# Kernel optimization log

Hardware: AMD Instinct MI355X
Metric: run time of the kernel (lower is better)

Reference implementation:

```python
import jax, jax.numpy as jnp
import numpy as np

N_ATOMS = 4096
MAX_ATOMS = 100
N_WEIGHTS = MAX_ATOMS * (MAX_ATOMS + 1) // 2  # 5050


def setup_inputs() -> dict:
    key = jax.random.key(0)
    k1, k2, k3, k4 = jax.random.split(key, 4)
    coordinates = jax.random.normal(k1, (N_ATOMS, 3), dtype=jnp.float32)
    atom_ix = jax.random.randint(k2, (N_ATOMS,), 0, MAX_ATOMS, dtype=jnp.int64)
    weights = jax.random.normal(k3, (N_WEIGHTS,), dtype=jnp.float32)
    bias = jax.random.normal(k4, (1,), dtype=jnp.float32)
    return {"coordinates": coordinates, "atom_ix": atom_ix, "weights": weights, "bias": bias}


def reference(coordinates, atom_ix, weights, bias):
    # diff: [N, N, 3]
    diff = coordinates[None, :, :] - coordinates[:, None, :]
    # torch.norm with no dim -> scalar Frobenius norm of the whole tensor
    d = jnp.sqrt(jnp.sum(diff * diff))
    # torch.nan_to_num(1/d, 0.0): nan->0, +inf->finfo.max (jnp defaults match)
    reciprocal_d = jnp.nan_to_num(1.0 / d, nan=0.0)
    # pairwise index into triangular weight table: [N, N]
    ai = atom_ix[:, None]
    pairwise_atom_ix = ai * (ai + 1) // 2 + atom_ix[None, :]
    atom_weights = weights[pairwise_atom_ix]  # gather -> [N, N]
    return jnp.sum(atom_weights * reciprocal_d) + bias  # shape (1,)
```

## Files before the change

### kernel.cpp

```cpp
#include <hip/hip_runtime.h>
#include <math.h>


#define NTHREADS 1024
#define N_WAVES (NTHREADS / 64)

constexpr int N_ATOMS   = 4096;
constexpr int MAX_ATOMS = 100;

__device__ __forceinline__ float waveReduceSum(float v) {
#pragma unroll
    for (int off = 32; off > 0; off >>= 1)
        v += __shfl_down(v, off, 64);
    return v;
}

__global__ __launch_bounds__(NTHREADS)
void SimpleEnergyModel_43903155700342_kernel(
        const float* __restrict__ coords,
        const int*   __restrict__ atom_ix,
        const float* __restrict__ weights,
        const float* __restrict__ bias,
        float*       __restrict__ out)
{
    __shared__ float    s_part[N_WAVES][4];
    __shared__ float    s_w[N_WAVES];
    __shared__ unsigned s_count[MAX_ATOMS];
    __shared__ float    s_cntf[MAX_ATOMS];

    const int tid  = threadIdx.x;
    const int lane = tid & 63;
    const int wave = tid >> 6;

    for (int t = tid; t < MAX_ATOMS; t += NTHREADS) s_count[t] = 0u;
    __syncthreads();

    float sumsq = 0.f, sx = 0.f, sy = 0.f, sz = 0.f;
    for (int i = tid; i < N_ATOMS; i += NTHREADS) {
        const float x = coords[3 * i + 0];
        const float y = coords[3 * i + 1];
        const float z = coords[3 * i + 2];
        sumsq = fmaf(x, x, sumsq);
        sumsq = fmaf(y, y, sumsq);
        sumsq = fmaf(z, z, sumsq);
        sx += x; sy += y; sz += z;
        atomicAdd(&s_count[atom_ix[i]], 1u);
    }
    sumsq = waveReduceSum(sumsq);
    sx    = waveReduceSum(sx);
    sy    = waveReduceSum(sy);
    sz    = waveReduceSum(sz);
    if (lane == 0) {
        s_part[wave][0] = sumsq;
        s_part[wave][1] = sx;
        s_part[wave][2] = sy;
        s_part[wave][3] = sz;
    }
    __syncthreads();

    for (int t = tid; t < MAX_ATOMS; t += NTHREADS) s_cntf[t] = (float)s_count[t];
    __syncthreads();

    float wsum = 0.f;
    for (int idx = tid; idx < MAX_ATOMS * MAX_ATOMS; idx += NTHREADS) {
        const int a = idx / MAX_ATOMS;
        const int b = idx - a * MAX_ATOMS;
        const float cc = s_cntf[a] * s_cntf[b];
        wsum = fmaf(cc, weights[(a * (a + 1)) / 2 + b], wsum);
    }
    wsum = waveReduceSum(wsum);
    if (lane == 0) s_w[wave] = wsum;
    __syncthreads();

    if (tid == 0) {
        float tss = 0.f, tx = 0.f, ty = 0.f, tz = 0.f, tw = 0.f;
#pragma unroll
        for (int w = 0; w < N_WAVES; ++w) {
            tss += s_part[w][0];
            tx  += s_part[w][1];
            ty  += s_part[w][2];
            tz  += s_part[w][3];
            tw  += s_w[w];
        }
        const float S = 2.f * (float)N_ATOMS * tss - 2.f * (tx * tx + ty * ty + tz * tz);
        const float d = sqrtf(S);
        const float rd = (d != 0.f) ? (1.f / d) : 0.f;
        out[0] = tw * rd + bias[0];
    }
}

extern "C" void kernel_launch(void* const* d_in, const int* in_sizes, int n_in,
                              void* d_out, int out_size, void* d_ws, size_t ws_size,
                              hipStream_t stream) {
    const float* coords  = (const float*)d_in[0];
    const int*   atom_ix = (const int*)  d_in[1];
    const float* weights = (const float*)d_in[2];
    const float* bias    = (const float*)d_in[3];
    float*       out     = (float*)d_out;

    SimpleEnergyModel_43903155700342_kernel<<<1, NTHREADS, 0, stream>>>(
        coords, atom_ix, weights, bias, out);
}
```

Baseline: 9.763 us.

## Prefetch weight table into registers and vectorize coordinate and index loads

All ten weight-table gathers per thread are issued up front into registers, before the count histogram and coordinate reduction. This overlaps their global-memory latency with the other loads instead of leaving it after a barrier. Coordinates are read as three float4 per thread, with the x/y/z component of each lane resolved by modular arithmetic, and atom indices are read as one int4. The final cross-wave reduction uses wave shuffles instead of a serial loop on one thread, and an extra barrier plus the float count array are removed. The code now hard-wires the sizes (4096 atoms, 1024 threads, 10000 pairs) and assumes 16-byte-aligned inputs, and it raises register use.

```diff
diff --git a/kernel.cpp b/kernel.cpp
--- a/kernel.cpp
+++ b/kernel.cpp
@@ -7,6 +7,7 @@
 
 constexpr int N_ATOMS   = 4096;
 constexpr int MAX_ATOMS = 100;
+constexpr int NPAIRS    = MAX_ATOMS * MAX_ATOMS;
 
 __device__ __forceinline__ float waveReduceSum(float v) {
 #pragma unroll
@@ -26,66 +27,101 @@
     __shared__ float    s_part[N_WAVES][4];
     __shared__ float    s_w[N_WAVES];
     __shared__ unsigned s_count[MAX_ATOMS];
-    __shared__ float    s_cntf[MAX_ATOMS];
 
     const int tid  = threadIdx.x;
     const int lane = tid & 63;
     const int wave = tid >> 6;
 
-    for (int t = tid; t < MAX_ATOMS; t += NTHREADS) s_count[t] = 0u;
+    const float bias0 = bias[0];
+
+    float wv[10];
+    int   wa[10], wb[10];
+#pragma unroll
+    for (int u = 0; u < 10; ++u) {
+        const int p = tid + u * NTHREADS;
+        if (p < NPAIRS) {
+            const int a = p / MAX_ATOMS;
+            const int b = p - a * MAX_ATOMS;
+            wa[u] = a; wb[u] = b;
+            wv[u] = weights[(a * (a + 1)) / 2 + b];
+        } else {
+            wa[u] = 0; wb[u] = 0; wv[u] = 0.f;
+        }
+    }
+
+    const float4* c4 = (const float4*)coords;
+    const float4 v0 = c4[tid];
+    const float4 v1 = c4[tid + NTHREADS];
+    const float4 v2 = c4[tid + 2 * NTHREADS];
+
+    const int4 ai = ((const int4*)atom_ix)[tid];
+
+    if (tid < MAX_ATOMS) s_count[tid] = 0u;
     __syncthreads();
+    atomicAdd(&s_count[ai.x], 1u);
+    atomicAdd(&s_count[ai.y], 1u);
+    atomicAdd(&s_count[ai.z], 1u);
+    atomicAdd(&s_count[ai.w], 1u);
 
-    float sumsq = 0.f, sx = 0.f, sy = 0.f, sz = 0.f;
-    for (int i = tid; i < N_ATOMS; i += NTHREADS) {
-        const float x = coords[3 * i + 0];
-        const float y = coords[3 * i + 1];
-        const float z = coords[3 * i + 2];
-        sumsq = fmaf(x, x, sumsq);
-        sumsq = fmaf(y, y, sumsq);
-        sumsq = fmaf(z, z, sumsq);
-        sx += x; sy += y; sz += z;
-        atomicAdd(&s_count[atom_ix[i]], 1u);
+    float sumsq = 0.f, c0 = 0.f, c1 = 0.f, c2 = 0.f;
+#pragma unroll
+    for (int u = 0; u < 3; ++u) {
+        const float4 v = (u == 0) ? v0 : (u == 1) ? v1 : v2;
+        const int r = (tid + u) % 3;
+        sumsq = fmaf(v.x, v.x, sumsq);
+        sumsq = fmaf(v.y, v.y, sumsq);
+        sumsq = fmaf(v.z, v.z, sumsq);
+        sumsq = fmaf(v.w, v.w, sumsq);
+        const float xw = v.x + v.w;
+        c0 += (r == 0) ? xw  : ((r == 1) ? v.z : v.y);
+        c1 += (r == 0) ? v.y : ((r == 1) ? xw  : v.z);
+        c2 += (r == 0) ? v.z : ((r == 1) ? v.y : xw);
     }
     sumsq = waveReduceSum(sumsq);
-    sx    = waveReduceSum(sx);
-    sy    = waveReduceSum(sy);
-    sz    = waveReduceSum(sz);
+    c0    = waveReduceSum(c0);
+    c1    = waveReduceSum(c1);
+    c2    = waveReduceSum(c2);
     if (lane == 0) {
         s_part[wave][0] = sumsq;
-        s_part[wave][1] = sx;
-        s_part[wave][2] = sy;
-        s_part[wave][3] = sz;
+        s_part[wave][1] = c0;
+        s_part[wave][2] = c1;
+        s_part[wave][3] = c2;
     }
     __syncthreads();
 
-    for (int t = tid; t < MAX_ATOMS; t += NTHREADS) s_cntf[t] = (float)s_count[t];
-    __syncthreads();
-
     float wsum = 0.f;
-    for (int idx = tid; idx < MAX_ATOMS * MAX_ATOMS; idx += NTHREADS) {
-        const int a = idx / MAX_ATOMS;
-        const int b = idx - a * MAX_ATOMS;
-        const float cc = s_cntf[a] * s_cntf[b];
-        wsum = fmaf(cc, weights[(a * (a + 1)) / 2 + b], wsum);
+#pragma unroll
+    for (int u = 0; u < 10; ++u) {
+        const float cc = (float)s_count[wa[u]] * (float)s_count[wb[u]];
+        wsum = fmaf(cc, wv[u], wsum);
     }
     wsum = waveReduceSum(wsum);
     if (lane == 0) s_w[wave] = wsum;
     __syncthreads();
 
-    if (tid == 0) {
-        float tss = 0.f, tx = 0.f, ty = 0.f, tz = 0.f, tw = 0.f;
+    if (wave == 0) {
+        float ts = 0.f, tx = 0.f, ty = 0.f, tz = 0.f, tw = 0.f;
+        if (lane < N_WAVES) {
+            ts = s_part[lane][0];
+            tx = s_part[lane][1];
+            ty = s_part[lane][2];
+            tz = s_part[lane][3];
+            tw = s_w[lane];
+        }
 #pragma unroll
-        for (int w = 0; w < N_WAVES; ++w) {
-            tss += s_part[w][0];
-            tx  += s_part[w][1];
-            ty  += s_part[w][2];
-            tz  += s_part[w][3];
-            tw  += s_w[w];
+        for (int off = 8; off >= 1; off >>= 1) {
+            ts += __shfl_down(ts, off, 64);
+            tx += __shfl_down(tx, off, 64);
+            ty += __shfl_down(ty, off, 64);
+            tz += __shfl_down(tz, off, 64);
+            tw += __shfl_down(tw, off, 64);
         }
-        const float S = 2.f * (float)N_ATOMS * tss - 2.f * (tx * tx + ty * ty + tz * tz);
-        const float d = sqrtf(S);
-        const float rd = (d != 0.f) ? (1.f / d) : 0.f;
-        out[0] = tw * rd + bias[0];
+        if (lane == 0) {
+            const float S = 2.f * (float)N_ATOMS * ts - 2.f * (tx * tx + ty * ty + tz * tz);
+            const float d = sqrtf(S);
+            const float rd = (d != 0.f) ? (1.f / d) : 0.f;
+            out[0] = tw * rd + bias0;
+        }
     }
 }
 
```

Measured after the change: 9.696 us. About the same (-0.7%).
